# Optimization experiments

Hardware: AMD Instinct MI355X
Metric: run time of the kernel (lower is better)

Reference implementation:

```python
import jax, jax.numpy as jnp
import numpy as np

R, C, E, H = 64, 2048, 128, 8  # num_rows(cells), num_cols(genes), embed_dim, heads
HD = E // H

def setup_inputs() -> dict:
    key = jax.random.key(0)
    ks = jax.random.split(key, 7)
    s = 1.0 / np.sqrt(E)
    return {
        "x": jax.random.normal(ks[0], (R, C, E), dtype=jnp.float32),
        "Wq": jax.random.normal(ks[1], (E, E), dtype=jnp.float32) * s,
        "bq": jax.random.normal(ks[2], (E,), dtype=jnp.float32) * 0.01,
        "Wk": jax.random.normal(ks[3], (E, E), dtype=jnp.float32) * s,
        "bk": jax.random.normal(ks[4], (E,), dtype=jnp.float32) * 0.01,
        "Wv": jax.random.normal(ks[5], (E, E), dtype=jnp.float32) * s,
        "bv": jax.random.normal(ks[6], (E,), dtype=jnp.float32) * 0.01,
    }

def reference(x, Wq, bq, Wk, bk, Wv, bv):
    num_rows, num_cols, embed_dim = x.shape
    head_dim = embed_dim // H

    def proj(W, b):
        # (R,C,E) -> (R,C,H,hd) -> (H,C,R,hd)
        y = (x @ W.T + b).reshape(num_rows, num_cols, H, head_dim)
        return jnp.transpose(y, (2, 1, 0, 3))

    q = proj(Wq, bq)
    k = proj(Wk, bk)
    v = proj(Wv, bv)

    # softmax over head_dim for q (before flattening rows into features)
    q = jax.nn.softmax(q, axis=-1).reshape(H, num_cols, num_rows * head_dim)
    k = k.reshape(H, num_cols, num_rows * head_dim)
    v = v.reshape(H, num_cols, num_rows * head_dim)

    dim = q.shape[-1]  # num_rows * head_dim
    k = jax.nn.softmax(k, axis=-2)      # softmax over sequence (num_cols)
    q = q * (dim ** -0.5)

    attn_weights = jnp.einsum('hnd,hmd->hnm', q, k)   # (H, C, C)
    context = jnp.einsum('hnd,hne->hde', k, v)        # (H, D, D)
    out = jnp.einsum('hnd,hde->hne', q, context)      # (H, C, D)

    out = out.reshape(H, num_cols, num_rows, head_dim)
    out = jnp.transpose(out, (2, 1, 0, 3)).reshape(num_rows, num_cols, embed_dim)
    return (out, attn_weights)
```

## Files before the change

kernel.cpp:

```cpp
#include <hip/hip_runtime.h>
#include <hip/hip_bf16.h>
#include <stdint.h>

typedef unsigned short u16;
typedef __attribute__((ext_vector_type(8))) short s16x8;
typedef __attribute__((ext_vector_type(4))) float f32x4;

__device__ __forceinline__ u16 f2bf(float f) {
    union { float f; uint32_t u; } v; v.f = f;
    uint32_t r = v.u + 0x7fffu + ((v.u >> 16) & 1u);
    return (u16)(r >> 16);
}
__device__ __forceinline__ float bf2f(u16 b) {
    union { uint32_t u; float f; } v; v.u = ((uint32_t)b) << 16;
    return v.f;
}
__device__ __forceinline__ void split2(float f, u16& h, u16& l) {
    h = f2bf(f);
    l = f2bf(f - bf2f(h));
}

__device__ __forceinline__ void load_lds16(const void* g, void* l) {
    __builtin_amdgcn_global_load_lds(
        (const __attribute__((address_space(1))) unsigned int*)g,
        (__attribute__((address_space(3))) unsigned int*)l,
        16, 0, 0);
}

__global__ __launch_bounds__(256, 2)
void proj_kernel(const float* __restrict__ x,
                 const float* __restrict__ Wq, const float* __restrict__ bq,
                 const float* __restrict__ Wk, const float* __restrict__ bk,
                 const float* __restrict__ Wv, const float* __restrict__ bv,
                 u16* __restrict__ Qs, float* __restrict__ KTf, u16* __restrict__ VT)
{
    __shared__ u16 Xh[128 * 132], Xl[128 * 132];
    const int tid = threadIdx.x;
    const int i0 = blockIdx.x * 128;
    const int r  = i0 >> 11;
    const int c0 = i0 & 2047;

    {
        const int col = (tid & 31) * 4;
        const int rb  = tid >> 5;
        #pragma unroll
        for (int pp = 0; pp < 16; ++pp) {
            int row = pp * 8 + rb;
            float4 v = *(const float4*)(x + (size_t)(i0 + row) * 128 + col);
            ushort4 hi, lo;
            split2(v.x, hi.x, lo.x); split2(v.y, hi.y, lo.y);
            split2(v.z, hi.z, lo.z); split2(v.w, hi.w, lo.w);
            *(ushort4*)&Xh[row * 132 + col] = hi;
            *(ushort4*)&Xl[row * 132 + col] = lo;
        }
    }
    __syncthreads();

    const int lane = tid & 63;
    const int w = tid >> 6;
    const int wr = w >> 1, wc = w & 1;
    const int lr = lane & 15, kc = lane >> 4;
    const f32x4 fzero = {0.f, 0.f, 0.f, 0.f};

    const float* const Wp[3] = { Wq, Wk, Wv };
    const float* const bp[3] = { bq, bk, bv };

    #pragma unroll
    for (int p = 0; p < 3; ++p) {
        const float* W = Wp[p];

        f32x4 acc[4][4];
        #pragma unroll
        for (int m = 0; m < 4; ++m)
            #pragma unroll
            for (int n = 0; n < 4; ++n) acc[m][n] = fzero;

        #pragma unroll
        for (int k0 = 0; k0 < 128; k0 += 32) {
            s16x8 ah[4], al[4];
            #pragma unroll
            for (int m = 0; m < 4; ++m) {
                ah[m] = *(const s16x8*)&Xh[(wr*64 + m*16 + lr) * 132 + k0 + kc*8];
                al[m] = *(const s16x8*)&Xl[(wr*64 + m*16 + lr) * 132 + k0 + kc*8];
            }
            #pragma unroll
            for (int n = 0; n < 4; ++n) {
                const float* wp8 = W + (size_t)(wc*64 + n*16 + lr) * 128 + k0 + kc*8;
                float4 w0 = *(const float4*)wp8;
                float4 w1 = *(const float4*)(wp8 + 4);
                s16x8 bh, bl;
                {
                    u16 hh, ll;
                    split2(w0.x, hh, ll); bh[0] = (short)hh; bl[0] = (short)ll;
                    split2(w0.y, hh, ll); bh[1] = (short)hh; bl[1] = (short)ll;
                    split2(w0.z, hh, ll); bh[2] = (short)hh; bl[2] = (short)ll;
                    split2(w0.w, hh, ll); bh[3] = (short)hh; bl[3] = (short)ll;
                    split2(w1.x, hh, ll); bh[4] = (short)hh; bl[4] = (short)ll;
                    split2(w1.y, hh, ll); bh[5] = (short)hh; bl[5] = (short)ll;
                    split2(w1.z, hh, ll); bh[6] = (short)hh; bl[6] = (short)ll;
                    split2(w1.w, hh, ll); bh[7] = (short)hh; bl[7] = (short)ll;
                }
                #pragma unroll
                for (int m = 0; m < 4; ++m) {
                    acc[m][n] = __builtin_amdgcn_mfma_f32_16x16x32_bf16(ah[m], bh, acc[m][n], 0, 0, 0);
                    acc[m][n] = __builtin_amdgcn_mfma_f32_16x16x32_bf16(al[m], bh, acc[m][n], 0, 0, 0);
                    acc[m][n] = __builtin_amdgcn_mfma_f32_16x16x32_bf16(ah[m], bl, acc[m][n], 0, 0, 0);
                }
            }
        }

        float bvals[4];
        #pragma unroll
        for (int n = 0; n < 4; ++n) bvals[n] = bp[p][wc*64 + n*16 + lr];

        if (p == 0) {
            #pragma unroll
            for (int m = 0; m < 4; ++m) {
                #pragma unroll
                for (int n = 0; n < 4; ++n) {
                    const int h  = wc*4 + n;
                    const int cb = c0 + wr*64 + m*16 + kc*4;
                    #pragma unroll
                    for (int j = 0; j < 4; ++j) {
                        float v = acc[m][n][j] + bvals[n];
                        float mx = v;
                        #pragma unroll
                        for (int s = 8; s >= 1; s >>= 1)
                            mx = fmaxf(mx, __shfl_xor(mx, s, 16));
                        float e = __expf(v - mx);
                        float sm = e;
                        #pragma unroll
                        for (int s = 8; s >= 1; s >>= 1)
                            sm += __shfl_xor(sm, s, 16);
                        float o = e / sm * 0.03125f;
                        Qs[((size_t)h * 2048 + cb + j) * 1024 + r*16 + lr] = f2bf(o);
                    }
                }
            }
        } else if (p == 1) {
            #pragma unroll
            for (int m = 0; m < 4; ++m) {
                #pragma unroll
                for (int n = 0; n < 4; ++n) {
                    const int h  = wc*4 + n;
                    const int cb = c0 + wr*64 + m*16 + kc*4;
                    float4 pk;
                    pk.x = acc[m][n][0] + bvals[n];
                    pk.y = acc[m][n][1] + bvals[n];
                    pk.z = acc[m][n][2] + bvals[n];
                    pk.w = acc[m][n][3] + bvals[n];
                    *(float4*)&KTf[((size_t)(h*1024 + r*16 + lr)) * 2048 + cb] = pk;
                }
            }
        } else {
            #pragma unroll
            for (int m = 0; m < 4; ++m) {
                #pragma unroll
                for (int n = 0; n < 4; ++n) {
                    const int h  = wc*4 + n;
                    const int cb = c0 + wr*64 + m*16 + kc*4;
                    ushort4 pk;
                    pk.x = f2bf(acc[m][n][0] + bvals[n]);
                    pk.y = f2bf(acc[m][n][1] + bvals[n]);
                    pk.z = f2bf(acc[m][n][2] + bvals[n]);
                    pk.w = f2bf(acc[m][n][3] + bvals[n]);
                    *(ushort4*)&VT[((size_t)(h*1024 + r*16 + lr)) * 2048 + cb] = pk;
                }
            }
        }
    }
}

__global__ __launch_bounds__(256)
void ksm_kernel(const float* __restrict__ KTf, u16* __restrict__ KTsm)
{
    const float* p = KTf + (size_t)blockIdx.x * 2048;
    u16* o = KTsm + (size_t)blockIdx.x * 2048;
    const int t = threadIdx.x;
    float4 a = *(const float4*)(p + t * 8);
    float4 b = *(const float4*)(p + t * 8 + 4);
    float v[8] = {a.x, a.y, a.z, a.w, b.x, b.y, b.z, b.w};
    float mx = v[0];
    #pragma unroll
    for (int j = 1; j < 8; ++j) mx = fmaxf(mx, v[j]);
    #pragma unroll
    for (int s = 32; s >= 1; s >>= 1) mx = fmaxf(mx, __shfl_xor(mx, s, 64));
    __shared__ float redm[4], reds[4];
    const int w = t >> 6;
    if ((t & 63) == 0) redm[w] = mx;
    __syncthreads();
    mx = fmaxf(fmaxf(redm[0], redm[1]), fmaxf(redm[2], redm[3]));
    float e[8]; float sm = 0.f;
    #pragma unroll
    for (int j = 0; j < 8; ++j) { e[j] = __expf(v[j] - mx); sm += e[j]; }
    #pragma unroll
    for (int s = 32; s >= 1; s >>= 1) sm += __shfl_xor(sm, s, 64);
    if ((t & 63) == 0) reds[w] = sm;
    __syncthreads();
    sm = reds[0] + reds[1] + reds[2] + reds[3];
    const float inv = 1.f / sm;
    uint4 ov; u16* op = (u16*)&ov;
    #pragma unroll
    for (int j = 0; j < 8; ++j) op[j] = f2bf(e[j] * inv);
    *(uint4*)(o + t * 8) = ov;
}

__global__ __launch_bounds__(256)
void ktrans_kernel(const u16* __restrict__ KTsm, u16* __restrict__ Ksm)
{
    const int h  = blockIdx.z;
    const int d0 = blockIdx.y * 64;
    const int c0 = blockIdx.x * 64;
    __shared__ u16 tile[64][72];
    const int t = threadIdx.x;
    #pragma unroll
    for (int i = 0; i < 2; ++i) {
        int g = t + i * 256;
        int dr = g >> 3;
        int cc = (g & 7) * 8;
        uint4 val = *(const uint4*)(KTsm + ((size_t)(h * 1024 + d0 + dr)) * 2048 + c0 + cc);
        *(uint4*)&tile[dr][cc] = val;
    }
    __syncthreads();
    #pragma unroll
    for (int i = 0; i < 2; ++i) {
        int g = t + i * 256;
        int cr = g >> 3;
        int dc = (g & 7) * 8;
        uint4 ov; u16* op = (u16*)&ov;
        #pragma unroll
        for (int j = 0; j < 8; ++j) op[j] = tile[dc + j][cr];
        *(uint4*)(Ksm + ((size_t)(h * 2048 + c0 + cr)) * 1024 + d0 + dc) = ov;
    }
}

template<int MODE>
__global__ __launch_bounds__(256, 2)
void gemm_bt(const u16* __restrict__ Aall, const u16* __restrict__ Ball,
             float* __restrict__ outF, u16* __restrict__ outB,
             const int M, const int N, const int K)
{
    const int h  = blockIdx.z;
    const int m0 = blockIdx.y * 128;
    const int n0 = blockIdx.x * 128;
    const u16* A = Aall + (size_t)h * M * K;
    const u16* B = Ball + (size_t)h * N * K;
    __shared__ u16 As[128 * 32];
    __shared__ u16 Bs[128 * 32];
    const int tid = threadIdx.x;
    const int lane = tid & 63;
    const int w = tid >> 6;
    const int wr = w >> 1, wc = w & 1;
    const int lr = lane & 15, kc = lane >> 4;
    const f32x4 fzero = {0.f, 0.f, 0.f, 0.f};

    f32x4 acc[4][4];
    #pragma unroll
    for (int m = 0; m < 4; ++m)
        #pragma unroll
        for (int n = 0; n < 4; ++n) acc[m][n] = fzero;

    const int srow = tid >> 2;
    const int scol = (tid & 3) * 8;
    const u16* ga = A + (size_t)(m0 + srow) * K + scol;
    const u16* gb = B + (size_t)(n0 + srow) * K + scol;
    char* lA = (char*)As + tid * 16;
    char* lB = (char*)Bs + tid * 16;
    const size_t rstep = (size_t)64 * K;

    for (int k0 = 0; k0 < K; k0 += 32) {
        __syncthreads();
        load_lds16(ga,         lA);
        load_lds16(ga + rstep, lA + 4096);
        load_lds16(gb,         lB);
        load_lds16(gb + rstep, lB + 4096);
        ga += 32; gb += 32;
        __syncthreads();

        s16x8 a[4], b[4];
        #pragma unroll
        for (int m = 0; m < 4; ++m)
            a[m] = *(const s16x8*)((const char*)As + (((wr*64 + m*16 + lr) * 32) + kc*8) * 2);
        #pragma unroll
        for (int n = 0; n < 4; ++n)
            b[n] = *(const s16x8*)((const char*)Bs + (((wc*64 + n*16 + lr) * 32) + kc*8) * 2);
        #pragma unroll
        for (int m = 0; m < 4; ++m)
            #pragma unroll
            for (int n = 0; n < 4; ++n)
                acc[m][n] = __builtin_amdgcn_mfma_f32_16x16x32_bf16(a[m], b[n], acc[m][n], 0, 0, 0);
    }

    #pragma unroll
    for (int m = 0; m < 4; ++m) {
        #pragma unroll
        for (int n = 0; n < 4; ++n) {
            const int grow0 = m0 + wr*64 + m*16 + kc*4;
            const int gcol  = n0 + wc*64 + n*16 + lr;
            #pragma unroll
            for (int j = 0; j < 4; ++j) {
                const float v = acc[m][n][j];
                const int grow = grow0 + j;
                if (MODE == 0) {
                    outF[(size_t)h * M * N + (size_t)grow * N + gcol] = v;
                } else if (MODE == 1) {
                    outB[(size_t)h * M * N + (size_t)grow * N + gcol] = f2bf(v);
                } else {
                    const int rr = gcol >> 4, hd = gcol & 15;
                    outF[((size_t)rr * 2048 + grow) * 128 + h * 16 + hd] = v;
                }
            }
        }
    }
}

extern "C" void kernel_launch(void* const* d_in, const int* in_sizes, int n_in,
                              void* d_out, int out_size, void* d_ws, size_t ws_size,
                              hipStream_t stream)
{
    const float* x  = (const float*)d_in[0];
    const float* Wq = (const float*)d_in[1];
    const float* bq = (const float*)d_in[2];
    const float* Wk = (const float*)d_in[3];
    const float* bk = (const float*)d_in[4];
    const float* Wv = (const float*)d_in[5];
    const float* bv = (const float*)d_in[6];

    float* outT = (float*)d_out;
    float* attn = outT + (size_t)64 * 2048 * 128;

    u16* Qs   = (u16*)d_ws;
    u16* Ksm  = Qs + (size_t)8 * 2048 * 1024;
    u16* KTsm = (u16*)outT;
    u16*   VT  = (u16*)attn;
    u16*   CT  = VT + (size_t)8 * 1024 * 2048;
    float* KTf = (float*)(CT + (size_t)8 * 1024 * 1024);

    proj_kernel<<<1024, 256, 0, stream>>>(x, Wq, bq, Wk, bk, Wv, bv, Qs, KTf, VT);
    ksm_kernel<<<8192, 256, 0, stream>>>(KTf, KTsm);
    ktrans_kernel<<<dim3(32, 16, 8), 256, 0, stream>>>(KTsm, Ksm);
    gemm_bt<1><<<dim3(8, 8, 8),  256, 0, stream>>>(VT, KTsm, nullptr, CT, 1024, 1024, 2048);
    gemm_bt<2><<<dim3(8, 16, 8), 256, 0, stream>>>(Qs, CT, outT, nullptr, 2048, 1024, 1024);
    gemm_bt<0><<<dim3(16, 16, 8), 256, 0, stream>>>(Qs, Ksm, attn, nullptr, 2048, 2048, 1024);
}
```

Before: 564.6 us.

## Presplit weights, shrink projection tiles, deepen GEMM K-tile, swizzle blocks, nontemporal stores

A new pre-kernel splits Wq/Wk/Wv into bf16 hi/lo arrays once, so the projection kernel no longer re-splits weights per block. The projection kernel is halved to 64 rows per block, with a grid of 2048 and higher occupancy. The generic GEMM now stages a K-tile of 64 instead of 32 per sync, which halves barriers, and it remaps block indices so heads interleave. Its fp32 outputs are written with nontemporal stores. The costs are more LDS per GEMM block (32KB), an extra small launch, and reliance on workspace space after KTf for the split weights.

Measured after the change: 542.2 us. 4.0% less time.

```diff
diff --git a/kernel.cpp b/kernel.cpp
--- a/kernel.cpp
+++ b/kernel.cpp
@@ -27,16 +27,29 @@
         16, 0, 0);
 }
 
-__global__ __launch_bounds__(256, 2)
-void proj_kernel(const float* __restrict__ x,
-                 const float* __restrict__ Wq, const float* __restrict__ bq,
-                 const float* __restrict__ Wk, const float* __restrict__ bk,
-                 const float* __restrict__ Wv, const float* __restrict__ bv,
+__global__ __launch_bounds__(256)
+void wsplit_kernel(const float* __restrict__ Wq, const float* __restrict__ Wk,
+                   const float* __restrict__ Wv, u16* __restrict__ Wsp)
+{
+    const int i = blockIdx.x * 256 + threadIdx.x;
+    const int p = i >> 14;
+    const int j = i & 16383;
+    const float* W = (p == 0) ? Wq : (p == 1) ? Wk : Wv;
+    const float v = W[j];
+    u16 h, l; split2(v, h, l);
+    Wsp[(size_t)p * 32768 + j]         = h;
+    Wsp[(size_t)p * 32768 + 16384 + j] = l;
+}
+
+__global__ __launch_bounds__(256, 4)
+void proj_kernel(const float* __restrict__ x, const u16* __restrict__ Wsp,
+                 const float* __restrict__ bq, const float* __restrict__ bk,
+                 const float* __restrict__ bv,
                  u16* __restrict__ Qs, float* __restrict__ KTf, u16* __restrict__ VT)
 {
-    __shared__ u16 Xh[128 * 132], Xl[128 * 132];
+    __shared__ u16 Xh[64 * 132], Xl[64 * 132];
     const int tid = threadIdx.x;
-    const int i0 = blockIdx.x * 128;
+    const int i0 = blockIdx.x * 64;
     const int r  = i0 >> 11;
     const int c0 = i0 & 2047;
 
@@ -44,7 +57,7 @@
         const int col = (tid & 31) * 4;
         const int rb  = tid >> 5;
         #pragma unroll
-        for (int pp = 0; pp < 16; ++pp) {
+        for (int pp = 0; pp < 8; ++pp) {
             int row = pp * 8 + rb;
             float4 v = *(const float4*)(x + (size_t)(i0 + row) * 128 + col);
             ushort4 hi, lo;
@@ -62,46 +75,33 @@
     const int lr = lane & 15, kc = lane >> 4;
     const f32x4 fzero = {0.f, 0.f, 0.f, 0.f};
 
-    const float* const Wp[3] = { Wq, Wk, Wv };
     const float* const bp[3] = { bq, bk, bv };
 
     #pragma unroll
     for (int p = 0; p < 3; ++p) {
-        const float* W = Wp[p];
-
-        f32x4 acc[4][4];
-        #pragma unroll
-        for (int m = 0; m < 4; ++m)
+        const u16* Wh = Wsp + (size_t)p * 32768;
+
+        f32x4 acc[2][4];
+        #pragma unroll
+        for (int m = 0; m < 2; ++m)
             #pragma unroll
             for (int n = 0; n < 4; ++n) acc[m][n] = fzero;
 
         #pragma unroll
         for (int k0 = 0; k0 < 128; k0 += 32) {
-            s16x8 ah[4], al[4];
-            #pragma unroll
-            for (int m = 0; m < 4; ++m) {
-                ah[m] = *(const s16x8*)&Xh[(wr*64 + m*16 + lr) * 132 + k0 + kc*8];
-                al[m] = *(const s16x8*)&Xl[(wr*64 + m*16 + lr) * 132 + k0 + kc*8];
+            s16x8 ah[2], al[2];
+            #pragma unroll
+            for (int m = 0; m < 2; ++m) {
+                ah[m] = *(const s16x8*)&Xh[(wr*32 + m*16 + lr) * 132 + k0 + kc*8];
+                al[m] = *(const s16x8*)&Xl[(wr*32 + m*16 + lr) * 132 + k0 + kc*8];
             }
             #pragma unroll
             for (int n = 0; n < 4; ++n) {
-                const float* wp8 = W + (size_t)(wc*64 + n*16 + lr) * 128 + k0 + kc*8;
-                float4 w0 = *(const float4*)wp8;
-                float4 w1 = *(const float4*)(wp8 + 4);
-                s16x8 bh, bl;
-                {
-                    u16 hh, ll;
-                    split2(w0.x, hh, ll); bh[0] = (short)hh; bl[0] = (short)ll;
-                    split2(w0.y, hh, ll); bh[1] = (short)hh; bl[1] = (short)ll;
-                    split2(w0.z, hh, ll); bh[2] = (short)hh; bl[2] = (short)ll;
-                    split2(w0.w, hh, ll); bh[3] = (short)hh; bl[3] = (short)ll;
-                    split2(w1.x, hh, ll); bh[4] = (short)hh; bl[4] = (short)ll;
-                    split2(w1.y, hh, ll); bh[5] = (short)hh; bl[5] = (short)ll;
-                    split2(w1.z, hh, ll); bh[6] = (short)hh; bl[6] = (short)ll;
-                    split2(w1.w, hh, ll); bh[7] = (short)hh; bl[7] = (short)ll;
-                }
-                #pragma unroll
-                for (int m = 0; m < 4; ++m) {
+                const u16* wb = Wh + (wc*64 + n*16 + lr) * 128 + k0 + kc*8;
+                s16x8 bh = *(const s16x8*)wb;
+                s16x8 bl = *(const s16x8*)(wb + 16384);
+                #pragma unroll
+                for (int m = 0; m < 2; ++m) {
                     acc[m][n] = __builtin_amdgcn_mfma_f32_16x16x32_bf16(ah[m], bh, acc[m][n], 0, 0, 0);
                     acc[m][n] = __builtin_amdgcn_mfma_f32_16x16x32_bf16(al[m], bh, acc[m][n], 0, 0, 0);
                     acc[m][n] = __builtin_amdgcn_mfma_f32_16x16x32_bf16(ah[m], bl, acc[m][n], 0, 0, 0);
@@ -115,11 +115,11 @@
 
         if (p == 0) {
             #pragma unroll
-            for (int m = 0; m < 4; ++m) {
+            for (int m = 0; m < 2; ++m) {
                 #pragma unroll
                 for (int n = 0; n < 4; ++n) {
                     const int h  = wc*4 + n;
-                    const int cb = c0 + wr*64 + m*16 + kc*4;
+                    const int cb = c0 + wr*32 + m*16 + kc*4;
                     #pragma unroll
                     for (int j = 0; j < 4; ++j) {
                         float v = acc[m][n][j] + bvals[n];
@@ -139,11 +139,11 @@
             }
         } else if (p == 1) {
             #pragma unroll
-            for (int m = 0; m < 4; ++m) {
+            for (int m = 0; m < 2; ++m) {
                 #pragma unroll
                 for (int n = 0; n < 4; ++n) {
                     const int h  = wc*4 + n;
-                    const int cb = c0 + wr*64 + m*16 + kc*4;
+                    const int cb = c0 + wr*32 + m*16 + kc*4;
                     float4 pk;
                     pk.x = acc[m][n][0] + bvals[n];
                     pk.y = acc[m][n][1] + bvals[n];
@@ -154,11 +154,11 @@
             }
         } else {
             #pragma unroll
-            for (int m = 0; m < 4; ++m) {
+            for (int m = 0; m < 2; ++m) {
                 #pragma unroll
                 for (int n = 0; n < 4; ++n) {
                     const int h  = wc*4 + n;
-                    const int cb = c0 + wr*64 + m*16 + kc*4;
+                    const int cb = c0 + wr*32 + m*16 + kc*4;
                     ushort4 pk;
                     pk.x = f2bf(acc[m][n][0] + bvals[n]);
                     pk.y = f2bf(acc[m][n][1] + bvals[n]);
@@ -240,13 +240,18 @@
              float* __restrict__ outF, u16* __restrict__ outB,
              const int M, const int N, const int K)
 {
-    const int h  = blockIdx.z;
-    const int m0 = blockIdx.y * 128;
-    const int n0 = blockIdx.x * 128;
+    const int gx = gridDim.x, gy = gridDim.y;
+    const int perh = gx * gy;
+    int flat = blockIdx.x + gx * (blockIdx.y + gy * blockIdx.z);
+    flat = (flat & 7) * perh + (flat >> 3);
+    const int h   = flat / perh;
+    const int rem = flat - h * perh;
+    const int m0  = (rem / gx) * 128;
+    const int n0  = (rem % gx) * 128;
     const u16* A = Aall + (size_t)h * M * K;
     const u16* B = Ball + (size_t)h * N * K;
-    __shared__ u16 As[128 * 32];
-    __shared__ u16 Bs[128 * 32];
+    __shared__ u16 As[128 * 64];
+    __shared__ u16 Bs[128 * 64];
     const int tid = threadIdx.x;
     const int lane = tid & 63;
     const int w = tid >> 6;
@@ -260,35 +265,42 @@
         #pragma unroll
         for (int n = 0; n < 4; ++n) acc[m][n] = fzero;
 
-    const int srow = tid >> 2;
-    const int scol = (tid & 3) * 8;
+    const int srow = tid >> 3;
+    const int scol = (tid & 7) * 8;
     const u16* ga = A + (size_t)(m0 + srow) * K + scol;
     const u16* gb = B + (size_t)(n0 + srow) * K + scol;
     char* lA = (char*)As + tid * 16;
     char* lB = (char*)Bs + tid * 16;
-    const size_t rstep = (size_t)64 * K;
-
-    for (int k0 = 0; k0 < K; k0 += 32) {
+    const size_t rstep = (size_t)32 * K;
+
+    for (int k0 = 0; k0 < K; k0 += 64) {
         __syncthreads();
-        load_lds16(ga,         lA);
-        load_lds16(ga + rstep, lA + 4096);
-        load_lds16(gb,         lB);
-        load_lds16(gb + rstep, lB + 4096);
-        ga += 32; gb += 32;
+        load_lds16(ga,             lA);
+        load_lds16(ga +     rstep, lA + 4096);
+        load_lds16(ga + 2 * rstep, lA + 8192);
+        load_lds16(ga + 3 * rstep, lA + 12288);
+        load_lds16(gb,             lB);
+        load_lds16(gb +     rstep, lB + 4096);
+        load_lds16(gb + 2 * rstep, lB + 8192);
+        load_lds16(gb + 3 * rstep, lB + 12288);
+        ga += 64; gb += 64;
         __syncthreads();
 
-        s16x8 a[4], b[4];
-        #pragma unroll
-        for (int m = 0; m < 4; ++m)
-            a[m] = *(const s16x8*)((const char*)As + (((wr*64 + m*16 + lr) * 32) + kc*8) * 2);
-        #pragma unroll
-        for (int n = 0; n < 4; ++n)
-            b[n] = *(const s16x8*)((const char*)Bs + (((wc*64 + n*16 + lr) * 32) + kc*8) * 2);
-        #pragma unroll
-        for (int m = 0; m < 4; ++m)
+        #pragma unroll
+        for (int kk = 0; kk < 64; kk += 32) {
+            s16x8 a[4], b[4];
+            #pragma unroll
+            for (int m = 0; m < 4; ++m)
+                a[m] = *(const s16x8*)((const char*)As + (((wr*64 + m*16 + lr) * 64) + kk + kc*8) * 2);
             #pragma unroll
             for (int n = 0; n < 4; ++n)
-                acc[m][n] = __builtin_amdgcn_mfma_f32_16x16x32_bf16(a[m], b[n], acc[m][n], 0, 0, 0);
+                b[n] = *(const s16x8*)((const char*)Bs + (((wc*64 + n*16 + lr) * 64) + kk + kc*8) * 2);
+            #pragma unroll
+            for (int m = 0; m < 4; ++m)
+                #pragma unroll
+                for (int n = 0; n < 4; ++n)
+                    acc[m][n] = __builtin_amdgcn_mfma_f32_16x16x32_bf16(a[m], b[n], acc[m][n], 0, 0, 0);
+        }
     }
 
     #pragma unroll
@@ -302,12 +314,12 @@
                 const float v = acc[m][n][j];
                 const int grow = grow0 + j;
                 if (MODE == 0) {
-                    outF[(size_t)h * M * N + (size_t)grow * N + gcol] = v;
+                    __builtin_nontemporal_store(v, &outF[(size_t)h * M * N + (size_t)grow * N + gcol]);
                 } else if (MODE == 1) {
                     outB[(size_t)h * M * N + (size_t)grow * N + gcol] = f2bf(v);
                 } else {
                     const int rr = gcol >> 4, hd = gcol & 15;
-                    outF[((size_t)rr * 2048 + grow) * 128 + h * 16 + hd] = v;
+                    __builtin_nontemporal_store(v, &outF[((size_t)rr * 2048 + grow) * 128 + h * 16 + hd]);
                 }
             }
         }
@@ -335,8 +347,10 @@
     u16*   VT  = (u16*)attn;
     u16*   CT  = VT + (size_t)8 * 1024 * 2048;
     float* KTf = (float*)(CT + (size_t)8 * 1024 * 1024);
-
-    proj_kernel<<<1024, 256, 0, stream>>>(x, Wq, bq, Wk, bk, Wv, bv, Qs, KTf, VT);
+    u16*   Wsp = (u16*)(KTf + (size_t)8 * 1024 * 2048);
+
+    wsplit_kernel<<<192, 256, 0, stream>>>(Wq, Wk, Wv, Wsp);
+    proj_kernel<<<2048, 256, 0, stream>>>(x, Wsp, bq, bk, bv, Qs, KTf, VT);
     ksm_kernel<<<8192, 256, 0, stream>>>(KTf, KTsm);
     ktrans_kernel<<<dim3(32, 16, 8), 256, 0, stream>>>(KTsm, Ksm);
     gemm_bt<1><<<dim3(8, 8, 8),  256, 0, stream>>>(VT, KTsm, nullptr, CT, 1024, 1024, 2048);
```
